# Optimization experiments

Hardware: AMD Instinct MI355X
Metric: run time of the kernel (lower is better)

Reference implementation:

```python
import jax, jax.numpy as jnp
import numpy as np

B, T, C = 2, 2048, 2048
N_HEAD, N_KV_HEAD = 16, 4
HEAD_DIM = C // N_HEAD  # 128
EPS = 1e-6


def rms_norm(x):
    # no learned scale, normalize over head_dim (last axis)
    return x * jax.lax.rsqrt(jnp.mean(jnp.square(x), axis=-1, keepdims=True) + EPS)


def apply_rotary_emb(x, cos, sin):
    # x: [B, T, H, D]; cos/sin: [T, D/2]  (rotate-half RoPE)
    x1, x2 = jnp.split(x, 2, axis=-1)
    c = cos[None, :, None, :]
    s = sin[None, :, None, :]
    return jnp.concatenate([x1 * c - x2 * s, x1 * s + x2 * c], axis=-1)


def setup_inputs() -> dict:
    key = jax.random.key(0)
    ks = jax.random.split(key, 6)
    x = jax.random.normal(ks[0], (B, T, C), dtype=jnp.float32)
    # real rotary tables: theta = 10000^{-2i/D}
    inv_freq = 1.0 / (10000.0 ** (jnp.arange(0, HEAD_DIM, 2, dtype=jnp.float32) / HEAD_DIM))
    angles = jnp.arange(T, dtype=jnp.float32)[:, None] * inv_freq[None, :]  # [T, D/2]
    cos, sin = jnp.cos(angles), jnp.sin(angles)
    std = 0.02
    Wq = jax.random.normal(ks[1], (C, N_HEAD * HEAD_DIM), dtype=jnp.float32) * std
    Wk = jax.random.normal(ks[2], (C, N_KV_HEAD * HEAD_DIM), dtype=jnp.float32) * std
    Wv = jax.random.normal(ks[3], (C, N_KV_HEAD * HEAD_DIM), dtype=jnp.float32) * std
    Wp = jax.random.normal(ks[4], (C, C), dtype=jnp.float32) * std
    return {"x": x, "cos": cos, "sin": sin, "Wq": Wq, "Wk": Wk, "Wv": Wv, "Wp": Wp}


def reference(x, cos, sin, Wq, Wk, Wv, Wp):
    Bx, Tx, Cx = x.shape
    q = (x @ Wq).reshape(Bx, Tx, N_HEAD, HEAD_DIM)
    k = (x @ Wk).reshape(Bx, Tx, N_KV_HEAD, HEAD_DIM)
    v = (x @ Wv).reshape(Bx, Tx, N_KV_HEAD, HEAD_DIM)
    q = rms_norm(apply_rotary_emb(q, cos, sin))
    k = rms_norm(apply_rotary_emb(k, cos, sin))
    # module scales q by 1/sqrt(D) AND nn.dot_product_attention scales again
    q = q * (1.0 / jnp.sqrt(HEAD_DIM))
    # GQA head repeat
    n_rep = N_HEAD // N_KV_HEAD
    k = jnp.repeat(k, n_rep, axis=2)  # [B, T, H, D]
    v = jnp.repeat(v, n_rep, axis=2)
    scores = jnp.einsum("bthd,bshd->bhts", q, k) / jnp.sqrt(jnp.asarray(HEAD_DIM, x.dtype))
    causal = jnp.tril(jnp.ones((Tx, Tx), dtype=bool))  # key <= query
    scores = jnp.where(causal[None, None, :, :], scores, jnp.finfo(scores.dtype).min)
    probs = jax.nn.softmax(scores, axis=-1)
    y = jnp.einsum("bhts,bshd->bthd", probs, v).reshape(Bx, Tx, Cx)
    return y @ Wp
```

## Files before the change

### kernel.cpp

```cpp
#include <hip/hip_runtime.h>
#include <hip/hip_bf16.h>
#include <math.h>

#define B_  2
#define T_  2048
#define C_  2048
#define NH_ 16
#define NKV_ 4
#define HD_ 128
#define NREP_ (NH_/NKV_)

#define QKVLD 3072
#define KOFF  2048
#define VOFF  2560

#define QSCALE 0.01127105500694502f

#if defined(__has_builtin)
# if __has_builtin(__builtin_amdgcn_exp2f)
#  define EXP2F(x) __builtin_amdgcn_exp2f(x)
# else
#  define EXP2F(x) exp2f(x)
# endif
#else
# define EXP2F(x) exp2f(x)
#endif

typedef __bf16 bf16x8 __attribute__((ext_vector_type(8)));
typedef float  f32x4  __attribute__((ext_vector_type(4)));
typedef float  f32x16 __attribute__((ext_vector_type(16)));

__device__ inline void gload_lds16(const void* g, void* l) {
    __builtin_amdgcn_global_load_lds((const __attribute__((address_space(1))) void*)g,
                                     (__attribute__((address_space(3))) void*)l, 16, 0, 0);
}

__global__ __launch_bounds__(256) void prep(const float* __restrict__ x,
                                            const float* __restrict__ Wq,
                                            const float* __restrict__ Wk,
                                            const float* __restrict__ Wv,
                                            const float* __restrict__ Wp,
                                            __bf16* __restrict__ xb,
                                            __bf16* __restrict__ wqkvT,
                                            __bf16* __restrict__ wpT)
{
    __shared__ float tl[32][33];
    const int bx  = blockIdx.x;
    const int tid = threadIdx.x;

    if (bx < 4096) {
        size_t i = ((size_t)bx * 256 + tid) * 8;
        float4 a = *(const float4*)&x[i];
        float4 b = *(const float4*)&x[i + 4];
        union { __bf16 h[8]; uint4 u; } pk;
        pk.h[0] = (__bf16)a.x; pk.h[1] = (__bf16)a.y; pk.h[2] = (__bf16)a.z; pk.h[3] = (__bf16)a.w;
        pk.h[4] = (__bf16)b.x; pk.h[5] = (__bf16)b.y; pk.h[6] = (__bf16)b.z; pk.h[7] = (__bf16)b.w;
        *(uint4*)&xb[i] = pk.u;
        return;
    }

    const float* src;
    int ncols, c0, dr0, k0;
    if (bx < 10240) {
        int r  = bx - 4096;
        int ct = r % 96;
        k0 = (r / 96) * 32;
        if (ct < 64)      { src = Wq; ncols = 2048; c0 = ct * 32;        dr0 = ct * 32; }
        else if (ct < 80) { src = Wk; ncols = 512;  c0 = (ct - 64) * 32; dr0 = KOFF + (ct - 64) * 32; }
        else              { src = Wv; ncols = 512;  c0 = (ct - 80) * 32; dr0 = VOFF + (ct - 80) * 32; }
    } else {
        int r  = bx - 10240;
        src = Wp; ncols = 2048;
        c0  = (r & 63) * 32; dr0 = c0;
        k0  = (r >> 6) * 32;
    }
    __bf16* dst = (bx < 10240) ? wqkvT : wpT;

    int rr = tid >> 3;
    int c4 = (tid & 7) * 4;
    float4 v = *(const float4*)&src[(size_t)(k0 + rr) * ncols + c0 + c4];
    tl[rr][c4] = v.x; tl[rr][c4 + 1] = v.y; tl[rr][c4 + 2] = v.z; tl[rr][c4 + 3] = v.w;
    __syncthreads();
    union { __bf16 h[4]; uint2 u; } pk;
#pragma unroll
    for (int j = 0; j < 4; ++j) pk.h[j] = (__bf16)tl[c4 + j][rr];
    *(uint2*)&dst[(size_t)(dr0 + rr) * 2048 + k0 + c4] = pk.u;
}

template<typename TOUT>
__global__ __launch_bounds__(256) void gemm_bt(const __bf16* __restrict__ A,
                                               const __bf16* __restrict__ Bt,
                                               TOUT* __restrict__ C,
                                               int M, int N, int K, int ldc)
{
    __shared__ __bf16 As[2][128 * 32];
    __shared__ __bf16 Bs[2][128 * 32];

    const int tid  = threadIdx.x;
    const int wv   = tid >> 6;
    const int lane = tid & 63;
    const int grp  = lane >> 4;
    const int id16 = lane & 15;
    const int wr   = wv >> 1;
    const int wc   = wv & 1;

    const int gx  = gridDim.x;
    const int nwg = gx * gridDim.y;
    const int q8  = nwg >> 3;
    const int lid = blockIdx.x + gx * blockIdx.y;
    const int swz = (lid & 7) * q8 + (lid >> 3);
    const int row0 = (swz / gx) * 128;
    const int col0 = (swz % gx) * 128;

    const int sm = tid >> 2;
    const int sk = (tid & 3) << 3;

    const __bf16* ga0 = A  + (size_t)(row0 + sm) * K + sk;
    const __bf16* ga1 = A  + (size_t)(row0 + 64 + sm) * K + sk;
    const __bf16* gb0 = Bt + (size_t)(col0 + sm) * K + sk;
    const __bf16* gb1 = Bt + (size_t)(col0 + 64 + sm) * K + sk;

    f32x4 acc[4][4];
    const f32x4 fz = {0.f, 0.f, 0.f, 0.f};
#pragma unroll
    for (int i = 0; i < 4; ++i)
#pragma unroll
        for (int j = 0; j < 4; ++j) acc[i][j] = fz;

    const int nk = K >> 5;

    {
        __bf16* a0 = &As[0][wv << 9];
        __bf16* b0 = &Bs[0][wv << 9];
        gload_lds16(ga0, a0);
        gload_lds16(ga1, a0 + 2048);
        gload_lds16(gb0, b0);
        gload_lds16(gb1, b0 + 2048);
    }

    for (int kt = 0; kt < nk; ++kt) {
        const int bufc = kt & 1;
        asm volatile("s_waitcnt vmcnt(0)" ::: "memory");
        __syncthreads();

        if (kt + 1 < nk) {
            const int kb = (kt + 1) << 5;
            __bf16* a0 = &As[1 - bufc][wv << 9];
            __bf16* b0 = &Bs[1 - bufc][wv << 9];
            gload_lds16(ga0 + kb, a0);
            gload_lds16(ga1 + kb, a0 + 2048);
            gload_lds16(gb0 + kb, b0);
            gload_lds16(gb1 + kb, b0 + 2048);
        }

        bf16x8 af[4], bfr[4];
#pragma unroll
        for (int i = 0; i < 4; ++i)
            af[i] = *(const bf16x8*)&As[bufc][((wr << 6) + (i << 4) + id16) * 32 + (grp << 3)];
#pragma unroll
        for (int j = 0; j < 4; ++j)
            bfr[j] = *(const bf16x8*)&Bs[bufc][((wc << 6) + (j << 4) + id16) * 32 + (grp << 3)];
#pragma unroll
        for (int i = 0; i < 4; ++i)
#pragma unroll
            for (int j = 0; j < 4; ++j)
                acc[i][j] = __builtin_amdgcn_mfma_f32_16x16x32_bf16(af[i], bfr[j], acc[i][j], 0, 0, 0);
    }

#pragma unroll
    for (int i = 0; i < 4; ++i) {
        int gr = row0 + (wr << 6) + (i << 4) + (grp << 2);
#pragma unroll
        for (int j = 0; j < 4; ++j) {
            int gc = col0 + (wc << 6) + (j << 4) + id16;
#pragma unroll
            for (int r = 0; r < 4; ++r) {
                if constexpr (sizeof(TOUT) == 4)
                    C[(size_t)(gr + r) * ldc + gc] = acc[i][j][r];
                else
                    C[(size_t)(gr + r) * ldc + gc] = (TOUT)acc[i][j][r];
            }
        }
    }
}

__global__ __launch_bounds__(256) void rope_vt(__bf16* __restrict__ qkv,
                                               const float* __restrict__ cosb,
                                               const float* __restrict__ sinb,
                                               __bf16* __restrict__ vt)
{
    __shared__ __bf16 tl[32][HD_ + 8];
    const int bx  = blockIdx.x;
    const int tid = threadIdx.x;

    if (bx < 20480) {
        int gw   = bx * 4 + (tid >> 6);
        int lane = tid & 63;
        int bt = gw / 20;
        int hd = gw % 20;
        int t  = bt & (T_ - 1);
        float scale = (hd < 16) ? QSCALE : 1.0f;

        __bf16* p = qkv + (size_t)bt * QKVLD + hd * HD_;
        float c = cosb[t * 64 + lane];
        float s = sinb[t * 64 + lane];
        float x1 = (float)p[lane];
        float x2 = (float)p[lane + 64];
        float r1 = x1 * c - x2 * s;
        float r2 = x1 * s + x2 * c;
        float ss = r1 * r1 + r2 * r2;
#pragma unroll
        for (int off = 32; off; off >>= 1) ss += __shfl_xor(ss, off, 64);
        float inv = rsqrtf(ss * (1.f / 128.f) + 1e-6f) * scale;
        p[lane]      = (__bf16)(r1 * inv);
        p[lane + 64] = (__bf16)(r2 * inv);
        return;
    }
    {
        int vbx = bx - 20480;
        int st  = vbx & 63;
        int bkv = vbx >> 6;
        int b = bkv >> 2, kv = bkv & 3;
        int s0 = st << 5;
        {
            int s = tid >> 3;
            int d = (tid & 7) << 4;
            const __bf16* src = qkv + (size_t)(b * T_ + s0 + s) * QKVLD + VOFF + kv * HD_ + d;
            *(bf16x8*)&tl[s][d]     = *(const bf16x8*)src;
            *(bf16x8*)&tl[s][d + 8] = *(const bf16x8*)(src + 8);
        }
        __syncthreads();
        {
            int d  = tid >> 1;
            int sh = (tid & 1) << 4;
            __bf16 tmp[16];
#pragma unroll
            for (int j = 0; j < 16; ++j) tmp[j] = tl[sh + j][d];
            __bf16* dst = vt + ((size_t)(b * NKV_ + kv) * HD_ + d) * T_ + s0 + sh;
            *(bf16x8*)dst       = *(bf16x8*)&tmp[0];
            *(bf16x8*)(dst + 8) = *(bf16x8*)&tmp[8];
        }
    }
}

__global__ __launch_bounds__(256, 2) void attn32(const __bf16* __restrict__ qkv,
                                                 const __bf16* __restrict__ vbT,
                                                 __bf16* __restrict__ y,
                                                 float* __restrict__ pOA,
                                                 float* __restrict__ pOB,
                                                 float* __restrict__ pLA,
                                                 float* __restrict__ pLB)
{
    __shared__ __bf16 Ks[2][64 * 128];
    __shared__ __bf16 Vs[2][64 * 128];

    const int tid  = threadIdx.x;
    const int wv   = tid >> 6;
    const int lane = tid & 63;
    const int l31  = lane & 31;
    const int h32  = lane >> 5;

    const int bx   = blockIdx.x;
    const int b    = (bx >> 2) & 1;
    const int kv   = bx & 3;
    const int m    = bx >> 3;
    const int hh   = m & 3;
    const int role = (m >> 2) & 1;
    const int p    = m >> 3;
    const int h    = kv * 4 + hh;
    const int bh   = b * 16 + h;
    const int slot = p * 32 + bh;

    const int hi  = 15 - p;
    const int lo  = p;
    const int tts = role ? (15 - 2 * p) : 99;

    auto KT = [&](int t) { return role ? (t < tts ? 17 + t : t - tts) : t; };

    int qw0 = hi * 128 + wv * 32;
    int qme = qw0 + l31;

    uint koff[4], voff[4];
#pragma unroll
    for (int i = 0; i < 4; ++i) {
        int r  = (wv * 4 + i) * 4 + (lane >> 4);
        int c  = lane & 15;
        int cs = c ^ (r & 15);
        koff[i] = (uint)(r * (QKVLD * 2) + cs * 16);
        int d   = r + ((cs >> 3) << 6);
        voff[i] = (uint)(d * (T_ * 2) + (cs & 7) * 16);
    }
    const char* kg = (const char*)(qkv + (size_t)b * T_ * QKVLD + KOFF + kv * HD_);
    const char* vg = (const char*)(vbT + ((size_t)(b * NKV_ + kv) * HD_) * T_);

    uint off8[8];
#pragma unroll
    for (int s = 0; s < 8; ++s)
        off8[s] = (uint)(l31 * 256 + ((((s << 1) + h32) ^ (l31 & 15)) << 4));

#define STAGE(BUF, KN)                                                        \
    {                                                                         \
        const char* kp = kg + (size_t)(KN) * (64 * QKVLD * 2);                \
        const char* vp = vg + (size_t)(KN) * (64 * 2);                        \
        __bf16* kl = &Ks[BUF][(wv * 4) * 512];                                \
        __bf16* vl = &Vs[BUF][(wv * 4) * 512];                                \
        _Pragma("unroll")                                                     \
        for (int i = 0; i < 4; ++i) gload_lds16(kp + koff[i], kl + i * 512);  \
        _Pragma("unroll")                                                     \
        for (int i = 0; i < 4; ++i) gload_lds16(vp + voff[i], vl + i * 512);  \
    }

    bf16x8 qf[8], qf2[8];
    {
        const __bf16* qp = qkv + (size_t)(b * T_ + hi * 128 + wv * 32 + l31) * QKVLD + h * HD_ + h32 * 8;
#pragma unroll
        for (int s = 0; s < 8; ++s) qf[s] = *(const bf16x8*)(qp + s * 16);
        const __bf16* qp2 = qkv + (size_t)(b * T_ + lo * 128 + wv * 32 + l31) * QKVLD + h * HD_ + h32 * 8;
#pragma unroll
        for (int s = 0; s < 8; ++s) qf2[s] = *(const bf16x8*)(qp2 + s * 16);
    }

    f32x16 o[4];
#pragma unroll
    for (int dt = 0; dt < 4; ++dt)
#pragma unroll
        for (int r = 0; r < 16; ++r) o[dt][r] = 0.f;
    float l_p = 0.f;

#define STORE_PARTIAL(PO, PL)                                                   \
    {                                                                           \
        float lsum = l_p + __shfl_xor(l_p, 32, 64);                             \
        int qloc = wv * 32 + l31;                                               \
        float* po = (PO) + ((size_t)slot * 128 + qloc) * 128;                   \
        _Pragma("unroll")                                                       \
        for (int dt = 0; dt < 4; ++dt)                                          \
            _Pragma("unroll")                                                   \
            for (int g = 0; g < 4; ++g) {                                       \
                float4 f = {o[dt][4 * g + 0], o[dt][4 * g + 1],                 \
                            o[dt][4 * g + 2], o[dt][4 * g + 3]};                \
                *(float4*)&po[dt * 32 + 8 * g + 4 * h32] = f;                   \
            }                                                                   \
        if (h32 == 0) (PL)[slot * 128 + qloc] = lsum;                           \
    }

#define TILE_BODY(TT, BUFC)                                                     \
    {                                                                           \
        const int tt_ = (TT);                                                   \
        asm volatile("s_waitcnt vmcnt(0)" ::: "memory");                        \
        __syncthreads();                                                        \
        if (tt_ + 1 < 17) { int kn_ = KT(tt_ + 1); STAGE(1 - (BUFC), kn_); }    \
        if (role && tt_ == tts) {                                               \
            STORE_PARTIAL(pOB, pLB);                                            \
            _Pragma("unroll")                                                   \
            for (int dt = 0; dt < 4; ++dt)                                      \
                _Pragma("unroll")                                               \
                for (int r = 0; r < 16; ++r) o[dt][r] = 0.f;                    \
            l_p = 0.f;                                                          \
            _Pragma("unroll")                                                   \
            for (int s = 0; s < 8; ++s) qf[s] = qf2[s];                         \
            qw0 = lo * 128 + wv * 32;                                           \
            qme = qw0 + l31;                                                    \
        }                                                                       \
        const int s0 = KT(tt_) << 6;                                            \
        if (s0 <= qw0 + 31) {                                                   \
            const char* Kb = (const char*)&Ks[BUFC][0];                         \
            const char* Vb = (const char*)&Vs[BUFC][0];                         \
            f32x16 S0, S1;                                                      \
            _Pragma("unroll")                                                   \
            for (int r = 0; r < 16; ++r) { S0[r] = 0.f; S1[r] = 0.f; }          \
            __builtin_amdgcn_s_setprio(1);                                      \
            _Pragma("unroll")                                                   \
            for (int s = 0; s < 8; ++s) {                                       \
                bf16x8 kf0 = *(const bf16x8*)(Kb + off8[s]);                    \
                bf16x8 kf1 = *(const bf16x8*)(Kb + off8[s] + 8192);             \
                S0 = __builtin_amdgcn_mfma_f32_32x32x16_bf16(kf0, qf[s], S0, 0, 0, 0); \
                S1 = __builtin_amdgcn_mfma_f32_32x32x16_bf16(kf1, qf[s], S1, 0, 0, 0); \
            }                                                                   \
            __builtin_amdgcn_s_setprio(0);                                      \
            const bool domask = (s0 + 63 > qw0);                                \
            uint w[16];                                                         \
            _Pragma("unroll")                                                   \
            for (int i = 0; i < 8; ++i) {                                       \
                const int r0 = 2 * i;                                           \
                float e0 = EXP2F(S0[r0]);                                       \
                float e1 = EXP2F(S0[r0 + 1]);                                   \
                if (domask) {                                                   \
                    int k0 = s0 + (r0 & 3) + 8 * (r0 >> 2) + 4 * h32;           \
                    if (k0     > qme) e0 = 0.f;                                 \
                    if (k0 + 1 > qme) e1 = 0.f;                                 \
                }                                                               \
                l_p += e0 + e1;                                                 \
                union { __bf16 h2[2]; uint u; } pk;                             \
                pk.h2[0] = (__bf16)e0; pk.h2[1] = (__bf16)e1;                   \
                w[i] = pk.u;                                                    \
            }                                                                   \
            _Pragma("unroll")                                                   \
            for (int i = 0; i < 8; ++i) {                                       \
                const int r0 = 2 * i;                                           \
                float e0 = EXP2F(S1[r0]);                                       \
                float e1 = EXP2F(S1[r0 + 1]);                                   \
                if (domask) {                                                   \
                    int k0 = s0 + 32 + (r0 & 3) + 8 * (r0 >> 2) + 4 * h32;      \
                    if (k0     > qme) e0 = 0.f;                                 \
                    if (k0 + 1 > qme) e1 = 0.f;                                 \
                }                                                               \
                l_p += e0 + e1;                                                 \
                union { __bf16 h2[2]; uint u; } pk;                             \
                pk.h2[0] = (__bf16)e0; pk.h2[1] = (__bf16)e1;                   \
                w[8 + i] = pk.u;                                                \
            }                                                                   \
            union U8 { uint u[4]; bf16x8 v; };                                  \
            bf16x8 pf[4];                                                       \
            _Pragma("unroll")                                                   \
            for (int ks = 0; ks < 4; ++ks) {                                    \
                const int bsel = ((ks >> 1) << 3) + ((ks & 1) << 2);            \
                uint a0 = w[bsel],     b0 = w[bsel + 2];                        \
                uint a1 = w[bsel + 1], b1 = w[bsel + 3];                        \
                asm("v_permlane32_swap_b32 %0, %1" : "+v"(a0), "+v"(b0));       \
                asm("v_permlane32_swap_b32 %0, %1" : "+v"(a1), "+v"(b1));       \
                U8 t;                                                           \
                t.u[0] = a0; t.u[1] = a1; t.u[2] = b0; t.u[3] = b1;             \
                pf[ks] = t.v;                                                   \
            }                                                                   \
            __builtin_amdgcn_s_setprio(1);                                      \
            _Pragma("unroll")                                                   \
            for (int dt = 0; dt < 4; ++dt) {                                    \
                const int ab = (dt >> 1) << 2;                                  \
                const int hf = (dt & 1) * 8192;                                 \
                _Pragma("unroll")                                               \
                for (int ks = 0; ks < 4; ++ks) {                                \
                    bf16x8 vf = *(const bf16x8*)(Vb + off8[ab + ks] + hf);      \
                    o[dt] = __builtin_amdgcn_mfma_f32_32x32x16_bf16(vf, pf[ks], o[dt], 0, 0, 0); \
                }                                                               \
            }                                                                   \
            __builtin_amdgcn_s_setprio(0);                                      \
        }                                                                       \
    }

    STAGE(0, KT(0));

    for (int tt = 0; tt < 16; tt += 2) {
        TILE_BODY(tt, 0);
        TILE_BODY(tt + 1, 1);
    }
    TILE_BODY(16, 0);

    if (role == 0) {
        STORE_PARTIAL(pOA, pLA);
    } else {
        float l  = l_p + __shfl_xor(l_p, 32, 64);
        float inv = 1.f / l;
        __bf16* yp = y + (size_t)(b * T_ + qw0 + l31) * C_ + h * HD_;
#pragma unroll
        for (int dt = 0; dt < 4; ++dt)
#pragma unroll
            for (int g = 0; g < 4; ++g) {
                union { __bf16 h4[4]; uint2 u; } pk;
#pragma unroll
                for (int e = 0; e < 4; ++e) pk.h4[e] = (__bf16)(o[dt][4 * g + e] * inv);
                *(uint2*)&yp[dt * 32 + 8 * g + 4 * h32] = pk.u;
            }
    }
#undef TILE_BODY
#undef STORE_PARTIAL
#undef STAGE
}

__global__ __launch_bounds__(256) void attn_combine(const float* __restrict__ pOA,
                                                    const float* __restrict__ pOB,
                                                    const float* __restrict__ pLA,
                                                    const float* __restrict__ pLB,
                                                    __bf16* __restrict__ y)
{
    int slot = blockIdx.x;
    int p  = slot >> 5, bh = slot & 31;
    int b  = bh >> 4,   h  = bh & 15;
    int hi = 15 - p;
    int t  = threadIdx.x;
    int q  = t >> 1;
    int dh = (t & 1) << 6;

    float inv = 1.f / (pLA[slot * 128 + q] + pLB[slot * 128 + q]);
    size_t base = ((size_t)slot * 128 + q) * 128 + dh;
    __bf16* yp = y + (size_t)(b * T_ + hi * 128 + q) * C_ + h * HD_ + dh;
#pragma unroll
    for (int d0 = 0; d0 < 64; d0 += 8) {
        float4 a0 = *(const float4*)&pOA[base + d0];
        float4 a1 = *(const float4*)&pOA[base + d0 + 4];
        float4 b0 = *(const float4*)&pOB[base + d0];
        float4 b1 = *(const float4*)&pOB[base + d0 + 4];
        union { __bf16 h8[8]; uint4 u; } pk;
        pk.h8[0] = (__bf16)((a0.x + b0.x) * inv);
        pk.h8[1] = (__bf16)((a0.y + b0.y) * inv);
        pk.h8[2] = (__bf16)((a0.z + b0.z) * inv);
        pk.h8[3] = (__bf16)((a0.w + b0.w) * inv);
        pk.h8[4] = (__bf16)((a1.x + b1.x) * inv);
        pk.h8[5] = (__bf16)((a1.y + b1.y) * inv);
        pk.h8[6] = (__bf16)((a1.z + b1.z) * inv);
        pk.h8[7] = (__bf16)((a1.w + b1.w) * inv);
        *(uint4*)&yp[d0] = pk.u;
    }
}

extern "C" void kernel_launch(void* const* d_in, const int* in_sizes, int n_in,
                              void* d_out, int out_size, void* d_ws, size_t ws_size,
                              hipStream_t stream)
{
    const float* x    = (const float*)d_in[0];
    const float* cosb = (const float*)d_in[1];
    const float* sinb = (const float*)d_in[2];
    const float* Wq   = (const float*)d_in[3];
    const float* Wk   = (const float*)d_in[4];
    const float* Wv   = (const float*)d_in[5];
    const float* Wp   = (const float*)d_in[6];
    float* out = (float*)d_out;

    const int M = B_ * T_;

    char* w = (char*)d_ws;
    __bf16* xb    = (__bf16*)w;  w += (size_t)M * C_ * 2;
    __bf16* qkv   = (__bf16*)w;  w += (size_t)M * QKVLD * 2;
    __bf16* wqkvT = (__bf16*)w;  w += (size_t)QKVLD * C_ * 2;
    __bf16* wpT   = (__bf16*)w;  w += (size_t)C_ * C_ * 2;
    __bf16* vt    = (__bf16*)w;  w += (size_t)M * NKV_ * HD_ * 2;
    __bf16* y     = (__bf16*)w;  w += (size_t)M * C_ * 2;
    float*  pOB   = (float*)w;
    float*  pOA   = (float*)xb;
    float*  pLA   = (float*)wqkvT;
    float*  pLB   = pLA + 8 * 32 * 128;

    prep<<<14336, 256, 0, stream>>>(x, Wq, Wk, Wv, Wp, xb, wqkvT, wpT);

    gemm_bt<__bf16><<<dim3(QKVLD / 128, M / 128), 256, 0, stream>>>(xb, wqkvT, qkv, M, QKVLD, C_, QKVLD);

    rope_vt<<<20992, 256, 0, stream>>>(qkv, cosb, sinb, vt);

    attn32<<<512, 256, 0, stream>>>(qkv, vt, y, pOA, pOB, pLA, pLB);
    attn_combine<<<256, 256, 0, stream>>>(pOA, pOB, pLA, pLB, y);

    gemm_bt<float><<<dim3(C_ / 128, M / 128), 256, 0, stream>>>(y, wpT, out, M, C_, C_, C_);
}
```

Measured before the change: 306.3 us.

## Fuse RoPE and RMSNorm into QKV GEMM epilogue, split V transpose kernel

The QKV GEMM now stages each 128-wide output tile (one head) in LDS as bf16 and applies rotary embedding, RMS normalization and the Q scale before writing to global memory. This removes a separate pass that re-read and re-wrote Q and K from global memory. The V transpose becomes its own small kernel. The epilogue adds serial per-row work inside the GEMM blocks and rounds to bf16 once more before RoPE.

```diff
diff --git a/kernel.cpp b/kernel.cpp
--- a/kernel.cpp
+++ b/kernel.cpp
@@ -87,14 +87,17 @@
     *(uint2*)&dst[(size_t)(dr0 + rr) * 2048 + k0 + c4] = pk.u;
 }
 
-template<typename TOUT>
+template<typename TOUT, bool QKV>
 __global__ __launch_bounds__(256) void gemm_bt(const __bf16* __restrict__ A,
                                                const __bf16* __restrict__ Bt,
                                                TOUT* __restrict__ C,
-                                               int M, int N, int K, int ldc)
+                                               int M, int N, int K, int ldc,
+                                               const float* __restrict__ cosb,
+                                               const float* __restrict__ sinb)
 {
-    __shared__ __bf16 As[2][128 * 32];
-    __shared__ __bf16 Bs[2][128 * 32];
+    __shared__ __bf16 smem[16384];
+#define ASP(b) (smem + (b) * 4096)
+#define BSP(b) (smem + 8192 + (b) * 4096)
 
     const int tid  = threadIdx.x;
     const int wv   = tid >> 6;
@@ -130,8 +133,8 @@
     const int nk = K >> 5;
 
     {
-        __bf16* a0 = &As[0][wv << 9];
-        __bf16* b0 = &Bs[0][wv << 9];
+        __bf16* a0 = ASP(0) + (wv << 9);
+        __bf16* b0 = BSP(0) + (wv << 9);
         gload_lds16(ga0, a0);
         gload_lds16(ga1, a0 + 2048);
         gload_lds16(gb0, b0);
@@ -145,8 +148,8 @@
 
         if (kt + 1 < nk) {
             const int kb = (kt + 1) << 5;
-            __bf16* a0 = &As[1 - bufc][wv << 9];
-            __bf16* b0 = &Bs[1 - bufc][wv << 9];
+            __bf16* a0 = ASP(1 - bufc) + (wv << 9);
+            __bf16* b0 = BSP(1 - bufc) + (wv << 9);
             gload_lds16(ga0 + kb, a0);
             gload_lds16(ga1 + kb, a0 + 2048);
             gload_lds16(gb0 + kb, b0);
@@ -156,15 +159,52 @@
         bf16x8 af[4], bfr[4];
 #pragma unroll
         for (int i = 0; i < 4; ++i)
-            af[i] = *(const bf16x8*)&As[bufc][((wr << 6) + (i << 4) + id16) * 32 + (grp << 3)];
+            af[i] = *(const bf16x8*)(ASP(bufc) + ((wr << 6) + (i << 4) + id16) * 32 + (grp << 3));
 #pragma unroll
         for (int j = 0; j < 4; ++j)
-            bfr[j] = *(const bf16x8*)&Bs[bufc][((wc << 6) + (j << 4) + id16) * 32 + (grp << 3)];
+            bfr[j] = *(const bf16x8*)(BSP(bufc) + ((wc << 6) + (j << 4) + id16) * 32 + (grp << 3));
 #pragma unroll
         for (int i = 0; i < 4; ++i)
 #pragma unroll
             for (int j = 0; j < 4; ++j)
                 acc[i][j] = __builtin_amdgcn_mfma_f32_16x16x32_bf16(af[i], bfr[j], acc[i][j], 0, 0, 0);
+    }
+
+    if constexpr (QKV) {
+        if (col0 < VOFF) {
+            __syncthreads();
+            __bf16 (*EB)[128] = (__bf16(*)[128])smem;
+#pragma unroll
+            for (int i = 0; i < 4; ++i)
+#pragma unroll
+                for (int j = 0; j < 4; ++j)
+#pragma unroll
+                    for (int r = 0; r < 4; ++r)
+                        EB[(wr << 6) + (i << 4) + (grp << 2) + r][(wc << 6) + (j << 4) + id16] =
+                            (__bf16)acc[i][j][r];
+            __syncthreads();
+
+            const float scale = (col0 < KOFF) ? QSCALE : 1.0f;
+            for (int ri = 0; ri < 32; ++ri) {
+                const int lrow = (wv << 5) + ri;
+                const int grow = row0 + lrow;
+                const int t = grow & (T_ - 1);
+                float c = cosb[t * 64 + lane];
+                float s = sinb[t * 64 + lane];
+                float x1 = (float)EB[lrow][lane];
+                float x2 = (float)EB[lrow][lane + 64];
+                float r1 = x1 * c - x2 * s;
+                float r2 = x1 * s + x2 * c;
+                float ss = r1 * r1 + r2 * r2;
+#pragma unroll
+                for (int off = 32; off; off >>= 1) ss += __shfl_xor(ss, off, 64);
+                float inv = rsqrtf(ss * (1.f / 128.f) + 1e-6f) * scale;
+                TOUT* qp = C + (size_t)grow * ldc + col0;
+                qp[lane]      = (TOUT)(r1 * inv);
+                qp[lane + 64] = (TOUT)(r2 * inv);
+            }
+            return;
+        }
     }
 
 #pragma unroll
@@ -182,64 +222,37 @@
             }
         }
     }
-}
-
-__global__ __launch_bounds__(256) void rope_vt(__bf16* __restrict__ qkv,
-                                               const float* __restrict__ cosb,
-                                               const float* __restrict__ sinb,
-                                               __bf16* __restrict__ vt)
+#undef ASP
+#undef BSP
+}
+
+__global__ __launch_bounds__(256) void vtrans(const __bf16* __restrict__ qkv,
+                                              __bf16* __restrict__ vt)
 {
     __shared__ __bf16 tl[32][HD_ + 8];
     const int bx  = blockIdx.x;
     const int tid = threadIdx.x;
-
-    if (bx < 20480) {
-        int gw   = bx * 4 + (tid >> 6);
-        int lane = tid & 63;
-        int bt = gw / 20;
-        int hd = gw % 20;
-        int t  = bt & (T_ - 1);
-        float scale = (hd < 16) ? QSCALE : 1.0f;
-
-        __bf16* p = qkv + (size_t)bt * QKVLD + hd * HD_;
-        float c = cosb[t * 64 + lane];
-        float s = sinb[t * 64 + lane];
-        float x1 = (float)p[lane];
-        float x2 = (float)p[lane + 64];
-        float r1 = x1 * c - x2 * s;
-        float r2 = x1 * s + x2 * c;
-        float ss = r1 * r1 + r2 * r2;
-#pragma unroll
-        for (int off = 32; off; off >>= 1) ss += __shfl_xor(ss, off, 64);
-        float inv = rsqrtf(ss * (1.f / 128.f) + 1e-6f) * scale;
-        p[lane]      = (__bf16)(r1 * inv);
-        p[lane + 64] = (__bf16)(r2 * inv);
-        return;
-    }
+    int st  = bx & 63;
+    int bkv = bx >> 6;
+    int b = bkv >> 2, kv = bkv & 3;
+    int s0 = st << 5;
     {
-        int vbx = bx - 20480;
-        int st  = vbx & 63;
-        int bkv = vbx >> 6;
-        int b = bkv >> 2, kv = bkv & 3;
-        int s0 = st << 5;
-        {
-            int s = tid >> 3;
-            int d = (tid & 7) << 4;
-            const __bf16* src = qkv + (size_t)(b * T_ + s0 + s) * QKVLD + VOFF + kv * HD_ + d;
-            *(bf16x8*)&tl[s][d]     = *(const bf16x8*)src;
-            *(bf16x8*)&tl[s][d + 8] = *(const bf16x8*)(src + 8);
-        }
-        __syncthreads();
-        {
-            int d  = tid >> 1;
-            int sh = (tid & 1) << 4;
-            __bf16 tmp[16];
-#pragma unroll
-            for (int j = 0; j < 16; ++j) tmp[j] = tl[sh + j][d];
-            __bf16* dst = vt + ((size_t)(b * NKV_ + kv) * HD_ + d) * T_ + s0 + sh;
-            *(bf16x8*)dst       = *(bf16x8*)&tmp[0];
-            *(bf16x8*)(dst + 8) = *(bf16x8*)&tmp[8];
-        }
+        int s = tid >> 3;
+        int d = (tid & 7) << 4;
+        const __bf16* src = qkv + (size_t)(b * T_ + s0 + s) * QKVLD + VOFF + kv * HD_ + d;
+        *(bf16x8*)&tl[s][d]     = *(const bf16x8*)src;
+        *(bf16x8*)&tl[s][d + 8] = *(const bf16x8*)(src + 8);
+    }
+    __syncthreads();
+    {
+        int d  = tid >> 1;
+        int sh = (tid & 1) << 4;
+        __bf16 tmp[16];
+#pragma unroll
+        for (int j = 0; j < 16; ++j) tmp[j] = tl[sh + j][d];
+        __bf16* dst = vt + ((size_t)(b * NKV_ + kv) * HD_ + d) * T_ + s0 + sh;
+        *(bf16x8*)dst       = *(bf16x8*)&tmp[0];
+        *(bf16x8*)(dst + 8) = *(bf16x8*)&tmp[8];
     }
 }
 
@@ -531,12 +544,14 @@
 
     prep<<<14336, 256, 0, stream>>>(x, Wq, Wk, Wv, Wp, xb, wqkvT, wpT);
 
-    gemm_bt<__bf16><<<dim3(QKVLD / 128, M / 128), 256, 0, stream>>>(xb, wqkvT, qkv, M, QKVLD, C_, QKVLD);
-
-    rope_vt<<<20992, 256, 0, stream>>>(qkv, cosb, sinb, vt);
+    gemm_bt<__bf16, true><<<dim3(QKVLD / 128, M / 128), 256, 0, stream>>>(
+        xb, wqkvT, qkv, M, QKVLD, C_, QKVLD, cosb, sinb);
+
+    vtrans<<<512, 256, 0, stream>>>(qkv, vt);
 
     attn32<<<512, 256, 0, stream>>>(qkv, vt, y, pOA, pOB, pLA, pLB);
     attn_combine<<<256, 256, 0, stream>>>(pOA, pOB, pLA, pLB, y);
 
-    gemm_bt<float><<<dim3(C_ / 128, M / 128), 256, 0, stream>>>(y, wpT, out, M, C_, C_, C_);
-}
+    gemm_bt<float, false><<<dim3(C_ / 128, M / 128), 256, 0, stream>>>(
+        y, wpT, out, M, C_, C_, C_, nullptr, nullptr);
+}
```

New measurement: 301.3 us. No clear change (-1.6%).
